# Optimization experiments

Measured on AMD Instinct MI355X. Metric: run time of the kernel, lower is better.

The kernel has to match this reference:

```python
import jax, jax.numpy as jnp
import numpy as np
from jax import lax

B, NC, NF = 16, 1024, 4096   # clouds, coarse pts/cloud, fine pts/cloud
C_IN, C_SKIP, C_HID, K = 256, 128, 256, 3
BN_EPS = 1e-5


def setup_inputs() -> dict:
    key = jax.random.key(0)
    ks = jax.random.split(key, 12)
    inp = {
        "x": jax.random.normal(ks[0], (B * NC, C_IN), jnp.float32),
        "pos": jax.random.normal(ks[1], (B * NC, 3), jnp.float32),
        "batch": jnp.arange(B * NC, dtype=jnp.int64) // NC,
        "x_skip": jax.random.normal(ks[2], (B * NF, C_SKIP), jnp.float32),
        "pos_skip": jax.random.normal(ks[3], (B * NF, 3), jnp.float32),
        "batch_skip": jnp.arange(B * NF, dtype=jnp.int64) // NF,
    }
    d_in = C_IN + C_SKIP
    inp["W1"] = jax.random.normal(ks[4], (d_in, C_HID), jnp.float32) / np.sqrt(d_in)
    inp["b1"] = jnp.zeros((C_HID,), jnp.float32)
    inp["g1"] = jnp.ones((C_HID,), jnp.float32)
    inp["be1"] = jnp.zeros((C_HID,), jnp.float32)
    inp["W2"] = jax.random.normal(ks[5], (C_HID, C_HID), jnp.float32) / np.sqrt(C_HID)
    inp["b2"] = jnp.zeros((C_HID,), jnp.float32)
    inp["g2"] = jnp.ones((C_HID,), jnp.float32)
    inp["be2"] = jnp.zeros((C_HID,), jnp.float32)
    return inp


def _knn_interpolate(x, pos, pos_skip):
    # batches are contiguous equal-size -> reshape per cloud
    xb = x.reshape(B, NC, C_IN)
    pc = pos.reshape(B, NC, 3)
    pf = pos_skip.reshape(B, NF, 3)
    # squared distances [B, NF, NC]
    d2 = jnp.sum((pf[:, :, None, :] - pc[:, None, :, :]) ** 2, axis=-1)
    neg_d, idx = lax.top_k(-d2, K)                      # [B, NF, K]
    w = 1.0 / jnp.maximum(-neg_d, 1e-16)                # inverse-squared-distance weights
    feats = xb[jnp.arange(B)[:, None, None], idx]       # [B, NF, K, C_IN]
    out = jnp.sum(w[..., None] * feats, axis=2) / jnp.sum(w, axis=2, keepdims=True)
    return out.reshape(B * NF, C_IN)


def _mlp_layer(h, W, b, g, be):
    z = jax.nn.relu(h @ W + b)
    mean = jnp.mean(z, axis=0)
    var = jnp.mean((z - mean) ** 2, axis=0)            # biased var, as torch BN
    return (z - mean) * lax.rsqrt(var + BN_EPS) * g + be


def reference(x, pos, batch, x_skip, pos_skip, batch_skip,
              W1, b1, g1, be1, W2, b2, g2, be2):
    h = _knn_interpolate(x, pos, pos_skip)
    h = jnp.concatenate([h, x_skip], axis=1)            # [B*NF, C_IN+C_SKIP]
    h = _mlp_layer(h, W1, b1, g1, be1)
    h = _mlp_layer(h, W2, b2, g2, be2)
    return h
```

## Files before the change

### kernel.cpp

```cpp
#include <hip/hip_runtime.h>
#include <hip/hip_bf16.h>

#define NB    16
#define NC    1024
#define NF    4096
#define MROWS 65536
#define CIN   256
#define CSK   128
#define DIN   384
#define CHID  256
#define BN_EPS 1e-5f

typedef __attribute__((ext_vector_type(8))) short bf16x8;
typedef __attribute__((ext_vector_type(4))) float f32x4;

__device__ __forceinline__ unsigned short f2bfu(float f) {
  __hip_bfloat16 h = __float2bfloat16(f);
  return __builtin_bit_cast(unsigned short, h);
}
__device__ __forceinline__ float bfu2f(unsigned short u) {
  unsigned int w = ((unsigned int)u) << 16;
  return __builtin_bit_cast(float, w);
}

__device__ __forceinline__ void load_lds16(const void* g, void* lds) {
  __builtin_amdgcn_global_load_lds(
      (const __attribute__((address_space(1))) unsigned int*)g,
      (__attribute__((address_space(3))) unsigned int*)lds, 16, 0, 0);
}

__global__ __launch_bounds__(256) void knn_interp_kernel(
    const float* __restrict__ x,
    const float* __restrict__ pos,
    const float* __restrict__ x_skip,
    const float* __restrict__ pos_skip,
    __hip_bfloat16* __restrict__ h0)
{
  __shared__ float4 cpos[NC];
  __shared__ float  md[4][64][3];
  __shared__ int    mi[4][64][3];
  __shared__ float  fw[64][3];
  __shared__ int    fi[64][3];

  const int tid = threadIdx.x, wid = tid >> 6, lane = tid & 63;
  const int f0 = blockIdx.x * 64;
  const int b  = f0 >> 12;

  const float* pb = pos + (size_t)b * NC * 3;
  for (int j = tid; j < NC; j += 256)
    cpos[j] = make_float4(pb[3 * j], pb[3 * j + 1], pb[3 * j + 2], 0.f);
  __syncthreads();

  const int f = f0 + lane;
  const float* pf = pos_skip + (size_t)f * 3;
  const float fx = pf[0], fy = pf[1], fz = pf[2];

  float b0 = 3.4e38f, b1 = 3.4e38f, b2v = 3.4e38f;
  int   i0 = 0, i1 = 0, i2 = 0;
  const int jbase = wid * 256;
#pragma unroll 4
  for (int jj = 0; jj < 256; ++jj) {
    const float4 c = cpos[jbase + jj];
    const float dx = __fsub_rn(fx, c.x);
    const float dy = __fsub_rn(fy, c.y);
    const float dz = __fsub_rn(fz, c.z);
    const float d2 = __fadd_rn(
        __fadd_rn(__fmul_rn(dx, dx), __fmul_rn(dy, dy)), __fmul_rn(dz, dz));
    const int j = jbase + jj;
    const bool c0 = d2 < b0, c1 = d2 < b1, c2 = d2 < b2v;
    const float nb1 = __builtin_amdgcn_fmed3f(d2, b0, b1);
    const float nb2 = __builtin_amdgcn_fmed3f(d2, b1, b2v);
    i2  = c1 ? i1 : (c2 ? j : i2);
    i1  = c0 ? i0 : (c1 ? j : i1);
    i0  = c0 ? j : i0;
    b2v = nb2;
    b1  = nb1;
    b0  = fminf(d2, b0);
  }
  md[wid][lane][0] = b0;  md[wid][lane][1] = b1;  md[wid][lane][2] = b2v;
  mi[wid][lane][0] = i0;  mi[wid][lane][1] = i1;  mi[wid][lane][2] = i2;
  __syncthreads();

  if (wid == 0) {
#pragma unroll
    for (int q = 1; q < 4; ++q) {
#pragma unroll
      for (int e = 0; e < 3; ++e) {
        const float d = md[q][lane][e];
        const int   j = mi[q][lane][e];
        const bool c0 = d < b0, c1 = d < b1, c2 = d < b2v;
        const float nb1 = __builtin_amdgcn_fmed3f(d, b0, b1);
        const float nb2 = __builtin_amdgcn_fmed3f(d, b1, b2v);
        i2  = c1 ? i1 : (c2 ? j : i2);
        i1  = c0 ? i0 : (c1 ? j : i1);
        i0  = c0 ? j : i0;
        b2v = nb2;
        b1  = nb1;
        b0  = fminf(d, b0);
      }
    }
    float w0 = 1.f / fmaxf(b0, 1e-16f);
    float w1 = 1.f / fmaxf(b1, 1e-16f);
    float w2 = 1.f / fmaxf(b2v, 1e-16f);
    const float inv = 1.f / (w0 + w1 + w2);
    fw[lane][0] = w0 * inv; fw[lane][1] = w1 * inv; fw[lane][2] = w2 * inv;
    fi[lane][0] = i0; fi[lane][1] = i1; fi[lane][2] = i2;
  }
  __syncthreads();

  for (int pp = 0; pp < 16; ++pp) {
    const int p = wid * 16 + pp;
    const float w0 = fw[p][0], w1 = fw[p][1], w2 = fw[p][2];
    const int j0 = fi[p][0], j1 = fi[p][1], j2 = fi[p][2];
    const float4* r0 = (const float4*)(x + (size_t)(b * NC + j0) * CIN);
    const float4* r1 = (const float4*)(x + (size_t)(b * NC + j1) * CIN);
    const float4* r2 = (const float4*)(x + (size_t)(b * NC + j2) * CIN);
    const float4 a0 = r0[lane], a1 = r1[lane], a2 = r2[lane];
    float4 v;
    v.x = w0 * a0.x + w1 * a1.x + w2 * a2.x;
    v.y = w0 * a0.y + w1 * a1.y + w2 * a2.y;
    v.z = w0 * a0.z + w1 * a1.z + w2 * a2.z;
    v.w = w0 * a0.w + w1 * a1.w + w2 * a2.w;
    __hip_bfloat16* orow = h0 + (size_t)(f0 + p) * DIN;
    ushort4 o;
    o.x = f2bfu(v.x); o.y = f2bfu(v.y); o.z = f2bfu(v.z); o.w = f2bfu(v.w);
    ((ushort4*)orow)[lane] = o;
    const float2 s = ((const float2*)(x_skip + (size_t)(f0 + p) * CSK))[lane];
    const unsigned int packed =
        ((unsigned int)f2bfu(s.y) << 16) | (unsigned int)f2bfu(s.x);
    ((unsigned int*)(orow + CIN))[lane] = packed;
  }
}

__global__ void prep_w1_kernel(const float* __restrict__ W1,
                               __hip_bfloat16* __restrict__ W1t,
                               float* __restrict__ stats) {
  int c = blockIdx.x, n = threadIdx.x;
  if (blockIdx.x == 0) {
    for (int k = threadIdx.x; k < 1024; k += 256) stats[k] = 0.f;
  }
  W1t[(size_t)n * DIN + c] = __float2bfloat16(W1[(size_t)c * CHID + n]);
}

__global__ void prep_w2_kernel(const float* __restrict__ W2,
                               const float* __restrict__ scale1,
                               __hip_bfloat16* __restrict__ W2t) {
  int c = blockIdx.x, n = threadIdx.x;
  W2t[(size_t)n * CHID + c] =
      __float2bfloat16(scale1[c] * W2[(size_t)c * CHID + n]);
}

__global__ __launch_bounds__(64) void prep_b2_kernel(
    const float* __restrict__ W2, const float* __restrict__ shift1,
    const float* __restrict__ b2, float* __restrict__ b2p) {
  const int n = blockIdx.x, l = threadIdx.x;
  float s = 0.f;
  for (int c = l; c < CHID; c += 64) s += shift1[c] * W2[(size_t)c * CHID + n];
#pragma unroll
  for (int off = 32; off > 0; off >>= 1) s += __shfl_down(s, off);
  if (l == 0) b2p[n] = s + b2[n];
}

template<int KD>
__global__ __launch_bounds__(256) void gemm_bias_relu(
    const __hip_bfloat16* __restrict__ A,
    const __hip_bfloat16* __restrict__ Bt,
    const float* __restrict__ bias,
    __hip_bfloat16* __restrict__ out,
    float* __restrict__ gsum,
    float* __restrict__ gsq)
{
  __shared__ __hip_bfloat16 As[128 * 32];
  __shared__ __hip_bfloat16 Bs[128 * 32];
  __shared__ float ssum[128], ssq[128];
  const int tid = threadIdx.x;
  const int wid = tid >> 6, lane = tid & 63;
  const int bid = blockIdx.x;
  const int bm = bid >> 1, bn = bid & 1;
  const int wr = wid >> 1, wc = wid & 1;
  const int la = lane & 15, lk = lane >> 4;

  if (tid < 128) { ssum[tid] = 0.f; ssq[tid] = 0.f; }

  f32x4 acc[4][4] = {};

  const int rA = tid >> 2;
  const int c8 = (tid & 3) * 8;
  const __hip_bfloat16* gA0 = A + (size_t)(bm * 128 + rA) * KD + c8;
  const __hip_bfloat16* gA1 = gA0 + (size_t)64 * KD;
  const __hip_bfloat16* gB0 = Bt + (size_t)(bn * 128 + rA) * KD + c8;
  const __hip_bfloat16* gB1 = gB0 + (size_t)64 * KD;
  char* ldsA = (char*)As + wid * 1024;
  char* ldsB = (char*)Bs + wid * 1024;

  const int nIter = KD / 32;
  for (int it = 0; it < nIter; ++it) {
    const int k0 = it * 32;
    load_lds16(gA0 + k0, ldsA);
    load_lds16(gA1 + k0, ldsA + 4096);
    load_lds16(gB0 + k0, ldsB);
    load_lds16(gB1 + k0, ldsB + 4096);
    __syncthreads();

    bf16x8 af[4], bfr[4];
#pragma unroll
    for (int m = 0; m < 4; ++m)
      af[m] = *(const bf16x8*)(As + (wr * 64 + m * 16 + la) * 32 + lk * 8);
#pragma unroll
    for (int n = 0; n < 4; ++n)
      bfr[n] = *(const bf16x8*)(Bs + (wc * 64 + n * 16 + la) * 32 + lk * 8);
#pragma unroll
    for (int m = 0; m < 4; ++m)
#pragma unroll
      for (int n = 0; n < 4; ++n)
        acc[m][n] = __builtin_amdgcn_mfma_f32_16x16x32_bf16(
            af[m], bfr[n], acc[m][n], 0, 0, 0);
    __syncthreads();
  }

  const int rowBase = bm * 128 + wr * 64 + lk * 4;
  const int lcolBase = wc * 64 + la;
#pragma unroll
  for (int n = 0; n < 4; ++n) {
    const int lcol = lcolBase + n * 16;
    const int col = bn * 128 + lcol;
    const float bs = bias[col];
    float ls = 0.f, ls2 = 0.f;
#pragma unroll
    for (int m = 0; m < 4; ++m) {
      const int row = rowBase + m * 16;
#pragma unroll
      for (int j = 0; j < 4; ++j) {
        float v = acc[m][n][j] + bs;
        v = fmaxf(v, 0.f);
        ls += v; ls2 += v * v;
        out[(size_t)(row + j) * 256 + col] = __float2bfloat16(v);
      }
    }
    atomicAdd(&ssum[lcol], ls);
    atomicAdd(&ssq[lcol], ls2);
  }
  __syncthreads();
  if (tid < 128) {
    atomicAdd(&gsum[bn * 128 + tid], ssum[tid]);
    atomicAdd(&gsq[bn * 128 + tid], ssq[tid]);
  }
}

__global__ void bn_finalize_kernel(const float* __restrict__ sum,
                                   const float* __restrict__ sumsq,
                                   const float* __restrict__ g,
                                   const float* __restrict__ be,
                                   float* __restrict__ scale,
                                   float* __restrict__ shift) {
  const int c = threadIdx.x;
  const float m = sum[c] * (1.f / MROWS);
  const float var = sumsq[c] * (1.f / MROWS) - m * m;
  const float sc = g[c] * rsqrtf(var + BN_EPS);
  scale[c] = sc;
  shift[c] = be[c] - m * sc;
}

__global__ __launch_bounds__(256) void bn_apply_kernel(
    const __hip_bfloat16* __restrict__ Z, const float* __restrict__ scale,
    const float* __restrict__ shift, float* __restrict__ out) {
  const size_t i8 = (size_t)blockIdx.x * 256 + threadIdx.x;
  const uint4 raw = ((const uint4*)Z)[i8];
  const int c0 = (int)((i8 * 8) & 255);
  const float4 scA = *(const float4*)(scale + c0);
  const float4 scB = *(const float4*)(scale + c0 + 4);
  const float4 shA = *(const float4*)(shift + c0);
  const float4 shB = *(const float4*)(shift + c0 + 4);
  float4 oa, ob;
  oa.x = bfu2f((unsigned short)(raw.x & 0xffff)) * scA.x + shA.x;
  oa.y = bfu2f((unsigned short)(raw.x >> 16))    * scA.y + shA.y;
  oa.z = bfu2f((unsigned short)(raw.y & 0xffff)) * scA.z + shA.z;
  oa.w = bfu2f((unsigned short)(raw.y >> 16))    * scA.w + shA.w;
  ob.x = bfu2f((unsigned short)(raw.z & 0xffff)) * scB.x + shB.x;
  ob.y = bfu2f((unsigned short)(raw.z >> 16))    * scB.y + shB.y;
  ob.z = bfu2f((unsigned short)(raw.w & 0xffff)) * scB.z + shB.z;
  ob.w = bfu2f((unsigned short)(raw.w >> 16))    * scB.w + shB.w;
  ((float4*)(out))[i8 * 2]     = oa;
  ((float4*)(out))[i8 * 2 + 1] = ob;
}

extern "C" void kernel_launch(void* const* d_in, const int* in_sizes, int n_in,
                              void* d_out, int out_size, void* d_ws,
                              size_t ws_size, hipStream_t stream) {
  (void)in_sizes; (void)n_in; (void)out_size; (void)ws_size;
  const float* x        = (const float*)d_in[0];
  const float* pos      = (const float*)d_in[1];
  const float* x_skip   = (const float*)d_in[3];
  const float* pos_skip = (const float*)d_in[4];
  const float* W1  = (const float*)d_in[6];
  const float* b1  = (const float*)d_in[7];
  const float* g1  = (const float*)d_in[8];
  const float* be1 = (const float*)d_in[9];
  const float* W2  = (const float*)d_in[10];
  const float* b2  = (const float*)d_in[11];
  const float* g2  = (const float*)d_in[12];
  const float* be2 = (const float*)d_in[13];
  float* out = (float*)d_out;

  char* ws = (char*)d_ws;
  __hip_bfloat16* h0  = (__hip_bfloat16*)(ws);
  __hip_bfloat16* z2  = (__hip_bfloat16*)(ws);
  __hip_bfloat16* W1t = (__hip_bfloat16*)(ws + 50331648);
  __hip_bfloat16* z1  = (__hip_bfloat16*)(ws + 50528256);
  __hip_bfloat16* W2t = (__hip_bfloat16*)(ws + 84082688);
  float* b2p    = (float*)(ws + 84213760);
  float* stats  = (float*)(ws + 84214784);
  float* scale1 = (float*)(ws + 84218880);
  float* shift1 = scale1 + 256;
  float* scale2 = scale1 + 512;
  float* shift2 = scale1 + 768;

  prep_w1_kernel<<<384, 256, 0, stream>>>(W1, W1t, stats);
  knn_interp_kernel<<<1024, 256, 0, stream>>>(x, pos, x_skip, pos_skip, h0);
  gemm_bias_relu<DIN><<<1024, 256, 0, stream>>>(h0, W1t, b1, z1,
                                                stats, stats + 256);
  bn_finalize_kernel<<<1, 256, 0, stream>>>(stats, stats + 256, g1, be1,
                                            scale1, shift1);
  prep_w2_kernel<<<256, 256, 0, stream>>>(W2, scale1, W2t);
  prep_b2_kernel<<<256, 64, 0, stream>>>(W2, shift1, b2, b2p);
  gemm_bias_relu<CHID><<<1024, 256, 0, stream>>>(z1, W2t, b2p, z2,
                                                 stats + 512, stats + 768);
  bn_finalize_kernel<<<1, 256, 0, stream>>>(stats + 512, stats + 768, g2, be2,
                                            scale2, shift2);
  bn_apply_kernel<<<8192, 256, 0, stream>>>(z2, scale2, shift2, out);
}
```

Measured before the change: 153.1 us.

## Fuse BN finalize into consumers and widen KNN blocks to 512 threads

The KNN kernel now runs 8 waves per block, each scanning 128 coarse points instead of 256, which shortens the serial top-3 scan per thread at the cost of a longer merge step in wave 0. The separate BN finalize kernels are removed: layer-1 finalize is folded into a merged W2-scaling and bias-folding kernel, and layer-2 finalize is recomputed per block inside bn_apply. This cuts four small launches and their serialization gaps, at the cost of redundant rsqrt work per block.

```diff
diff --git a/kernel.cpp b/kernel.cpp
--- a/kernel.cpp
+++ b/kernel.cpp
@@ -29,7 +29,7 @@
       (__attribute__((address_space(3))) unsigned int*)lds, 16, 0, 0);
 }
 
-__global__ __launch_bounds__(256) void knn_interp_kernel(
+__global__ __launch_bounds__(512) void knn_interp_kernel(
     const float* __restrict__ x,
     const float* __restrict__ pos,
     const float* __restrict__ x_skip,
@@ -37,8 +37,8 @@
     __hip_bfloat16* __restrict__ h0)
 {
   __shared__ float4 cpos[NC];
-  __shared__ float  md[4][64][3];
-  __shared__ int    mi[4][64][3];
+  __shared__ float  md[8][64][3];
+  __shared__ int    mi[8][64][3];
   __shared__ float  fw[64][3];
   __shared__ int    fi[64][3];
 
@@ -47,7 +47,7 @@
   const int b  = f0 >> 12;
 
   const float* pb = pos + (size_t)b * NC * 3;
-  for (int j = tid; j < NC; j += 256)
+  for (int j = tid; j < NC; j += 512)
     cpos[j] = make_float4(pb[3 * j], pb[3 * j + 1], pb[3 * j + 2], 0.f);
   __syncthreads();
 
@@ -57,9 +57,9 @@
 
   float b0 = 3.4e38f, b1 = 3.4e38f, b2v = 3.4e38f;
   int   i0 = 0, i1 = 0, i2 = 0;
-  const int jbase = wid * 256;
+  const int jbase = wid * 128;
 #pragma unroll 4
-  for (int jj = 0; jj < 256; ++jj) {
+  for (int jj = 0; jj < 128; ++jj) {
     const float4 c = cpos[jbase + jj];
     const float dx = __fsub_rn(fx, c.x);
     const float dy = __fsub_rn(fy, c.y);
@@ -83,7 +83,7 @@
 
   if (wid == 0) {
 #pragma unroll
-    for (int q = 1; q < 4; ++q) {
+    for (int q = 1; q < 8; ++q) {
 #pragma unroll
       for (int e = 0; e < 3; ++e) {
         const float d = md[q][lane][e];
@@ -108,8 +108,8 @@
   }
   __syncthreads();
 
-  for (int pp = 0; pp < 16; ++pp) {
-    const int p = wid * 16 + pp;
+  for (int pp = 0; pp < 8; ++pp) {
+    const int p = wid * 8 + pp;
     const float w0 = fw[p][0], w1 = fw[p][1], w2 = fw[p][2];
     const int j0 = fi[p][0], j1 = fi[p][1], j2 = fi[p][2];
     const float4* r0 = (const float4*)(x + (size_t)(b * NC + j0) * CIN);
@@ -142,23 +142,26 @@
   W1t[(size_t)n * DIN + c] = __float2bfloat16(W1[(size_t)c * CHID + n]);
 }
 
-__global__ void prep_w2_kernel(const float* __restrict__ W2,
-                               const float* __restrict__ scale1,
-                               __hip_bfloat16* __restrict__ W2t) {
-  int c = blockIdx.x, n = threadIdx.x;
-  W2t[(size_t)n * CHID + c] =
-      __float2bfloat16(scale1[c] * W2[(size_t)c * CHID + n]);
-}
-
-__global__ __launch_bounds__(64) void prep_b2_kernel(
-    const float* __restrict__ W2, const float* __restrict__ shift1,
-    const float* __restrict__ b2, float* __restrict__ b2p) {
-  const int n = blockIdx.x, l = threadIdx.x;
-  float s = 0.f;
-  for (int c = l; c < CHID; c += 64) s += shift1[c] * W2[(size_t)c * CHID + n];
-#pragma unroll
-  for (int off = 32; off > 0; off >>= 1) s += __shfl_down(s, off);
-  if (l == 0) b2p[n] = s + b2[n];
+__global__ __launch_bounds__(256) void prep_w2b2_kernel(
+    const float* __restrict__ W2, const float* __restrict__ stats,
+    const float* __restrict__ g1, const float* __restrict__ be1,
+    const float* __restrict__ b2, __hip_bfloat16* __restrict__ W2t,
+    float* __restrict__ b2p) {
+  const int n = blockIdx.x, c = threadIdx.x;
+  const int wid = c >> 6, lane = c & 63;
+  const float m = stats[c] * (1.f / MROWS);
+  const float var = stats[256 + c] * (1.f / MROWS) - m * m;
+  const float sc = g1[c] * rsqrtf(var + BN_EPS);
+  const float sh = be1[c] - m * sc;
+  const float w = W2[(size_t)c * CHID + n];
+  W2t[(size_t)n * CHID + c] = __float2bfloat16(sc * w);
+  float p = sh * w;
+#pragma unroll
+  for (int off = 32; off > 0; off >>= 1) p += __shfl_down(p, off);
+  __shared__ float red4[4];
+  if (lane == 0) red4[wid] = p;
+  __syncthreads();
+  if (c == 0) b2p[n] = red4[0] + red4[1] + red4[2] + red4[3] + b2[n];
 }
 
 template<int KD>
@@ -247,30 +250,27 @@
   }
 }
 
-__global__ void bn_finalize_kernel(const float* __restrict__ sum,
-                                   const float* __restrict__ sumsq,
-                                   const float* __restrict__ g,
-                                   const float* __restrict__ be,
-                                   float* __restrict__ scale,
-                                   float* __restrict__ shift) {
-  const int c = threadIdx.x;
-  const float m = sum[c] * (1.f / MROWS);
-  const float var = sumsq[c] * (1.f / MROWS) - m * m;
-  const float sc = g[c] * rsqrtf(var + BN_EPS);
-  scale[c] = sc;
-  shift[c] = be[c] - m * sc;
-}
-
 __global__ __launch_bounds__(256) void bn_apply_kernel(
-    const __hip_bfloat16* __restrict__ Z, const float* __restrict__ scale,
-    const float* __restrict__ shift, float* __restrict__ out) {
-  const size_t i8 = (size_t)blockIdx.x * 256 + threadIdx.x;
+    const __hip_bfloat16* __restrict__ Z, const float* __restrict__ stats,
+    const float* __restrict__ g2, const float* __restrict__ be2,
+    float* __restrict__ out) {
+  __shared__ float ssc[256], ssh[256];
+  const int t = threadIdx.x;
+  {
+    const float m = stats[t] * (1.f / MROWS);
+    const float var = stats[256 + t] * (1.f / MROWS) - m * m;
+    const float sc = g2[t] * rsqrtf(var + BN_EPS);
+    ssc[t] = sc;
+    ssh[t] = be2[t] - m * sc;
+  }
+  __syncthreads();
+  const size_t i8 = (size_t)blockIdx.x * 256 + t;
   const uint4 raw = ((const uint4*)Z)[i8];
   const int c0 = (int)((i8 * 8) & 255);
-  const float4 scA = *(const float4*)(scale + c0);
-  const float4 scB = *(const float4*)(scale + c0 + 4);
-  const float4 shA = *(const float4*)(shift + c0);
-  const float4 shB = *(const float4*)(shift + c0 + 4);
+  const float4 scA = *(const float4*)(ssc + c0);
+  const float4 scB = *(const float4*)(ssc + c0 + 4);
+  const float4 shA = *(const float4*)(ssh + c0);
+  const float4 shB = *(const float4*)(ssh + c0 + 4);
   float4 oa, ob;
   oa.x = bfu2f((unsigned short)(raw.x & 0xffff)) * scA.x + shA.x;
   oa.y = bfu2f((unsigned short)(raw.x >> 16))    * scA.y + shA.y;
@@ -310,22 +310,13 @@
   __hip_bfloat16* W2t = (__hip_bfloat16*)(ws + 84082688);
   float* b2p    = (float*)(ws + 84213760);
   float* stats  = (float*)(ws + 84214784);
-  float* scale1 = (float*)(ws + 84218880);
-  float* shift1 = scale1 + 256;
-  float* scale2 = scale1 + 512;
-  float* shift2 = scale1 + 768;
 
   prep_w1_kernel<<<384, 256, 0, stream>>>(W1, W1t, stats);
-  knn_interp_kernel<<<1024, 256, 0, stream>>>(x, pos, x_skip, pos_skip, h0);
+  knn_interp_kernel<<<1024, 512, 0, stream>>>(x, pos, x_skip, pos_skip, h0);
   gemm_bias_relu<DIN><<<1024, 256, 0, stream>>>(h0, W1t, b1, z1,
                                                 stats, stats + 256);
-  bn_finalize_kernel<<<1, 256, 0, stream>>>(stats, stats + 256, g1, be1,
-                                            scale1, shift1);
-  prep_w2_kernel<<<256, 256, 0, stream>>>(W2, scale1, W2t);
-  prep_b2_kernel<<<256, 64, 0, stream>>>(W2, shift1, b2, b2p);
+  prep_w2b2_kernel<<<256, 256, 0, stream>>>(W2, stats, g1, be1, b2, W2t, b2p);
   gemm_bias_relu<CHID><<<1024, 256, 0, stream>>>(z1, W2t, b2p, z2,
                                                  stats + 512, stats + 768);
-  bn_finalize_kernel<<<1, 256, 0, stream>>>(stats + 512, stats + 768, g2, be2,
-                                            scale2, shift2);
-  bn_apply_kernel<<<8192, 256, 0, stream>>>(z2, scale2, shift2, out);
-}
+  bn_apply_kernel<<<8192, 256, 0, stream>>>(z2, stats + 512, g2, be2, out);
+}
```

After: 147.9 us. -3.4%, faster.
